# Optimization experiments

Hardware: AMD Instinct MI355X
Metric: run time of the kernel (lower is better)

The kernel has to match this reference:

```python
import jax, jax.numpy as jnp
import numpy as np
import math

B, S, D, H, DQ, DV, P = 8, 1024, 512, 8, 64, 64, 32


def _layer_norm(x, g, b, eps=1e-5):
    mu = jnp.mean(x, axis=-1, keepdims=True)
    var = jnp.mean((x - mu) ** 2, axis=-1, keepdims=True)
    return (x - mu) * jax.lax.rsqrt(var + eps) * g + b


def setup_inputs() -> dict:
    key = jax.random.key(0)
    ks = jax.random.split(key, 12)
    s = 0.02
    x = jax.random.normal(ks[0], (B, S, D), dtype=jnp.float32)
    lengths = jax.random.randint(ks[1], (B,), S // 2, S + 1)  # avoid fully-masked rows
    return {
        "x": x,
        "ln_g": jnp.ones((D,), jnp.float32),
        "ln_b": jnp.zeros((D,), jnp.float32),
        "Wk": jax.random.normal(ks[2], (D, H * DQ), jnp.float32) * s,
        "bk": jnp.zeros((H * DQ,), jnp.float32),
        "Wv": jax.random.normal(ks[3], (D, H * DV), jnp.float32) * s,
        "bv": jnp.zeros((H * DV,), jnp.float32),
        "pos": jax.random.normal(ks[4], (1, S, S, P), jnp.float32) * s,  # learned pos table
        "wp": jax.random.normal(ks[5], (P,), jnp.float32) * s,  # map_pos Linear(P,1) weight
        "bp": jnp.zeros((), jnp.float32),  # map_pos bias
        "Wo": jax.random.normal(ks[6], (H * DV, D), jnp.float32) * s,
        "bo": jnp.zeros((D,), jnp.float32),
        "key_value_sequence_lengths": lengths,
    }


def reference(x, ln_g, ln_b, Wk, bk, Wv, bv, pos, wp, bp, Wo, bo, key_value_sequence_lengths):
    # self-attention, encoder (no causal mask), 'kv+pos' branch, eval mode (dropout off)
    xn = _layer_norm(x, ln_g, ln_b)
    k = (xn @ Wk + bk).reshape(B, S, H, DQ).transpose(0, 2, 1, 3)  # [B,H,S,DQ]
    v = (xn @ Wv + bv).reshape(B, S, H, DV).transpose(0, 2, 1, 3)  # [B,H,S,DV]

    # kv+pos: scores use keys twice (tmp = keys since N == M)
    scores = jnp.einsum("bhnd,bhmd->bhnm", k, k) / math.sqrt(H)
    # map_pos(scores[...,None] + pos) == scores * sum(wp) + pos@wp + bp (linear, fused)
    bias = jnp.einsum("qkp,p->qk", pos[0], wp) + bp  # [S,S]
    attn = scores * jnp.sum(wp) + bias[None, None]
    attn = attn / math.sqrt(DQ)

    key_ok = jnp.arange(S)[None, None, None, :] < key_value_sequence_lengths[:, None, None, None]
    attn = jnp.where(key_ok, attn, -jnp.inf)
    probs = jax.nn.softmax(attn, axis=-1)  # [B,H,S,S]

    out = jnp.einsum("bhnm,bhmd->bhnd", probs, v)
    out = out.transpose(0, 2, 1, 3).reshape(B, S, H * DV)
    seq = out @ Wo + bo + x
    return seq, probs
```

## Files before the change

kernel.cpp:

```cpp
#include <hip/hip_runtime.h>
#include <hip/hip_bf16.h>


typedef __attribute__((ext_vector_type(8))) short short8;
typedef __attribute__((ext_vector_type(4))) short short4v;
typedef __attribute__((ext_vector_type(4))) float float4v;

#define MFMA16(a, b, c) __builtin_amdgcn_mfma_f32_16x16x32_bf16((a), (b), (c), 0, 0, 0)

__device__ inline unsigned short f2bf(float f) {
    unsigned u = __builtin_bit_cast(unsigned, f);
    unsigned r = (u + 0x7FFFu + ((u >> 16) & 1u)) >> 16;
    return (unsigned short)r;
}
__device__ inline float bf2f(unsigned short h) {
    unsigned u = ((unsigned)h) << 16;
    return __builtin_bit_cast(float, u);
}

__device__ __forceinline__ void async16(const void* g, void* l) {
    __builtin_amdgcn_global_load_lds(
        (const __attribute__((address_space(1))) unsigned int*)(unsigned long long)g,
        (__attribute__((address_space(3))) unsigned int*)(unsigned)(unsigned long long)l,
        16, 0, 0);
}

__device__ __forceinline__ void barrier_lds() {
    asm volatile("s_waitcnt lgkmcnt(0)" ::: "memory");
    __builtin_amdgcn_sched_barrier(0);
    __builtin_amdgcn_s_barrier();
    __builtin_amdgcn_sched_barrier(0);
}

__global__ __launch_bounds__(256) void ln_kernel(const float* __restrict__ x,
                                                 const float* __restrict__ g,
                                                 const float* __restrict__ b,
                                                 unsigned short* __restrict__ xn) {
    int wave = threadIdx.x >> 6;
    int lane = threadIdx.x & 63;
    size_t row = (size_t)blockIdx.x * 4 + wave;
    const float4* x4 = (const float4*)(x + row * 512);
    float4 v0 = x4[lane];
    float4 v1 = x4[lane + 64];
    float s = v0.x + v0.y + v0.z + v0.w + v1.x + v1.y + v1.z + v1.w;
    for (int o = 32; o; o >>= 1) s += __shfl_xor(s, o);
    float mu = s * (1.0f / 512.0f);
    float d0x = v0.x - mu, d0y = v0.y - mu, d0z = v0.z - mu, d0w = v0.w - mu;
    float d1x = v1.x - mu, d1y = v1.y - mu, d1z = v1.z - mu, d1w = v1.w - mu;
    float q = d0x * d0x + d0y * d0y + d0z * d0z + d0w * d0w +
              d1x * d1x + d1y * d1y + d1z * d1z + d1w * d1w;
    for (int o = 32; o; o >>= 1) q += __shfl_xor(q, o);
    float rs = rsqrtf(q * (1.0f / 512.0f) + 1e-5f);
    const float4* g4 = (const float4*)g;
    const float4* b4 = (const float4*)b;
    float4 g0 = g4[lane], g1 = g4[lane + 64];
    float4 b0 = b4[lane], b1 = b4[lane + 64];
    short4v o0, o1;
    o0[0] = (short)f2bf(d0x * rs * g0.x + b0.x);
    o0[1] = (short)f2bf(d0y * rs * g0.y + b0.y);
    o0[2] = (short)f2bf(d0z * rs * g0.z + b0.z);
    o0[3] = (short)f2bf(d0w * rs * g0.w + b0.w);
    o1[0] = (short)f2bf(d1x * rs * g1.x + b1.x);
    o1[1] = (short)f2bf(d1y * rs * g1.y + b1.y);
    o1[2] = (short)f2bf(d1z * rs * g1.z + b1.z);
    o1[3] = (short)f2bf(d1w * rs * g1.w + b1.w);
    *(short4v*)(xn + row * 512 + lane * 4) = o0;
    *(short4v*)(xn + row * 512 + 256 + lane * 4) = o1;
}

__global__ __launch_bounds__(256) void wconv_kernel(const float* __restrict__ Wk,
                                                    const float* __restrict__ Wv,
                                                    const float* __restrict__ Wo,
                                                    unsigned short* __restrict__ WkT,
                                                    unsigned short* __restrict__ WvT,
                                                    unsigned short* __restrict__ WoT) {
    int i = blockIdx.x * 256 + threadIdx.x;
    const float* src = (blockIdx.y == 0) ? Wk : (blockIdx.y == 1) ? Wv : Wo;
    unsigned short* dst = (blockIdx.y == 0) ? WkT : (blockIdx.y == 1) ? WvT : WoT;
    int k = i >> 9, n = i & 511;
    dst[n * 512 + k] = f2bf(src[i]);
}

__global__ __launch_bounds__(256) void bias_kernel(const float* __restrict__ pos,
                                                   const float* __restrict__ wp,
                                                   const float* __restrict__ bp,
                                                   unsigned short* __restrict__ biasT) {
    int lane = threadIdx.x & 63;
    int w = threadIdx.x >> 6;
    size_t wbase = ((size_t)blockIdx.x * 4 + w) * 64;
    float4 wv = ((const float4*)wp)[lane & 7];
    float bias0 = bp[0];
#pragma unroll
    for (int t = 0; t < 8; t++) {
        size_t p0 = wbase + (size_t)t * 8;
        const float4* src = (const float4*)(pos + p0 * 32);
        float4 d = src[lane];
        float s = d.x * wv.x + d.y * wv.y + d.z * wv.z + d.w * wv.w;
        s += __shfl_xor(s, 1);
        s += __shfl_xor(s, 2);
        s += __shfl_xor(s, 4);
        if ((lane & 7) == 0) {
            size_t p = p0 + (lane >> 3);
            int q = (int)(p >> 10), k = (int)(p & 1023);
            biasT[(size_t)k * 1024 + q] = f2bf((s + bias0) * 0.125f);
        }
    }
}

__global__ __launch_bounds__(256) void proj_kernel(const unsigned short* __restrict__ xn,
                                                   const unsigned short* __restrict__ WkT,
                                                   const unsigned short* __restrict__ WvT,
                                                   const float* __restrict__ bk,
                                                   const float* __restrict__ bv,
                                                   unsigned short* __restrict__ K,
                                                   unsigned short* __restrict__ Vt) {
    __shared__ unsigned short sa[128 * 32];
    __shared__ unsigned short sb[128 * 32];
    int z = blockIdx.z;
    const unsigned short* Bm = z ? WvT : WkT;
    const float* bias = z ? bv : bk;
    int m0 = blockIdx.y * 128, n0 = blockIdx.x * 128;
    int lane = threadIdx.x & 63, w = threadIdx.x >> 6;
    int l15 = lane & 15, quad = lane >> 4, q8 = quad * 8;
    int wm = w >> 1, wn = w & 1;
    int srow = w * 16 + (lane >> 2);
    int scol = (lane & 3) * 8;
    float4v acc[4][4] = {};
    for (int k0 = 0; k0 < 512; k0 += 32) {
        __syncthreads();
        async16(xn + (size_t)(m0 + srow) * 512 + k0 + scol, &sa[w * 512]);
        async16(xn + (size_t)(m0 + 64 + srow) * 512 + k0 + scol, &sa[2048 + w * 512]);
        async16(Bm + (size_t)(n0 + srow) * 512 + k0 + scol, &sb[w * 512]);
        async16(Bm + (size_t)(n0 + 64 + srow) * 512 + k0 + scol, &sb[2048 + w * 512]);
        __syncthreads();
        short8 af[4], bf[4];
#pragma unroll
        for (int t = 0; t < 4; t++)
            af[t] = *(const short8*)&sa[(wm * 64 + t * 16 + l15) * 32 + q8];
#pragma unroll
        for (int t = 0; t < 4; t++)
            bf[t] = *(const short8*)&sb[(wn * 64 + t * 16 + l15) * 32 + q8];
#pragma unroll
        for (int mt = 0; mt < 4; mt++)
#pragma unroll
            for (int nt = 0; nt < 4; nt++)
                acc[mt][nt] = MFMA16(af[mt], bf[nt], acc[mt][nt]);
    }
#pragma unroll
    for (int mt = 0; mt < 4; mt++)
#pragma unroll
        for (int nt = 0; nt < 4; nt++)
#pragma unroll
            for (int r = 0; r < 4; r++) {
                int m = m0 + wm * 64 + mt * 16 + quad * 4 + r;
                int n = n0 + wn * 64 + nt * 16 + l15;
                float v = acc[mt][nt][r] + bias[n];
                int b = m >> 10, s = m & 1023;
                int h = n >> 6, d = n & 63;
                if (z == 0)
                    K[(((size_t)b * 8 + h) * 1024 + s) * 64 + d] = f2bf(v);
                else
                    Vt[(((size_t)b * 8 + h) * 64 + d) * 1024 + s] = f2bf(v);
            }
}

__global__ __launch_bounds__(256) void attn_kernel(const unsigned short* __restrict__ K,
                                                   const unsigned short* __restrict__ Vt,
                                                   const unsigned short* __restrict__ biasT,
                                                   const float* __restrict__ wp,
                                                   const int* __restrict__ lens,
                                                   float* __restrict__ probs,
                                                   unsigned short* __restrict__ outb) {
    __shared__ unsigned short sc[16 * 1032];
    int bid = blockIdx.x;
    int sup = bid >> 6, wi = bid & 63;
    int bh = (sup & ~7) | (wi >> 3);
    int qt = ((sup & 7) << 3) | (wi & 7);
    int b = bh >> 3, h = bh & 7;
    int q0 = qt * 16;
    int lane = threadIdx.x & 63;
    int w = threadIdx.x >> 6;
    int l15 = lane & 15, quad = lane >> 4;
    int q8 = quad * 8;
    int len = lens[b];

    float swp = 0.f;
#pragma unroll
    for (int j = 0; j < 32; j++) swp += wp[j];
    float c1 = swp * 0.04419417382415922f;

    const unsigned short* Kbh = K + (size_t)bh * 1024 * 64;
    short8 a00 = *(const short8*)(Kbh + (size_t)(q0 + l15) * 64 + q8);
    short8 a01 = *(const short8*)(Kbh + (size_t)(q0 + l15) * 64 + q8 + 32);

#pragma unroll 2
    for (int i = 0; i < 16; i++) {
        int n0 = (i * 4 + w) * 16;
        short8 b0 = *(const short8*)(Kbh + (size_t)(n0 + l15) * 64 + q8);
        short8 b1 = *(const short8*)(Kbh + (size_t)(n0 + l15) * 64 + q8 + 32);
        float4v acc0 = {};
        acc0 = MFMA16(a00, b0, acc0);
        acc0 = MFMA16(a01, b1, acc0);
        int key = n0 + l15;
        bool ok = key < len;
        short4v bb4 = *(const short4v*)(biasT + (size_t)key * 1024 + q0 + quad * 4);
#pragma unroll
        for (int r = 0; r < 4; r++) {
            int row0 = quad * 4 + r;
            float lg0 = ok ? acc0[r] * c1 + bf2f((unsigned short)bb4[r]) : -1e30f;
            sc[row0 * 1032 + key] = f2bf(lg0);
        }
    }
    barrier_lds();

    for (int rr = 0; rr < 4; rr++) {
        int row = w * 4 + rr;
        float v[16];
        float mx = -1e30f;
#pragma unroll
        for (int j = 0; j < 16; j++) {
            v[j] = bf2f(sc[row * 1032 + lane + j * 64]);
            mx = fmaxf(mx, v[j]);
        }
        for (int o = 32; o; o >>= 1) mx = fmaxf(mx, __shfl_xor(mx, o));
        float s = 0.f;
#pragma unroll
        for (int j = 0; j < 16; j++) {
            v[j] = __expf(v[j] - mx);
            s += v[j];
        }
        for (int o = 32; o; o >>= 1) s += __shfl_xor(s, o);
        float inv = 1.0f / s;
        float* prow = probs + ((size_t)bh * 1024 + q0 + row) * 1024;
#pragma unroll
        for (int j = 0; j < 16; j++) {
            float p = v[j] * inv;
            sc[row * 1032 + lane + j * 64] = f2bf(p);
            __builtin_nontemporal_store(p, prow + lane + j * 64);
        }
    }
    barrier_lds();

    int nv = w * 16;
    const unsigned short* Vbh = Vt + (size_t)bh * 64 * 1024;
    float4v o0a = {}, o0b = {};
    for (int ks = 0; ks < 32; ks += 2) {
        int k0 = ks * 32;
        short8 bb0 = *(const short8*)(Vbh + (size_t)(nv + l15) * 1024 + k0 + q8);
        short8 p0 = *(const short8*)&sc[l15 * 1032 + k0 + q8];
        short8 bb1 = *(const short8*)(Vbh + (size_t)(nv + l15) * 1024 + k0 + 32 + q8);
        short8 p1 = *(const short8*)&sc[l15 * 1032 + k0 + 32 + q8];
        o0a = MFMA16(p0, bb0, o0a);
        o0b = MFMA16(p1, bb1, o0b);
    }
    float4v o0 = o0a + o0b;
#pragma unroll
    for (int r = 0; r < 4; r++) {
        int row = quad * 4 + r;
        int qa = q0 + row;
        outb[((size_t)b * 1024 + qa) * 512 + h * 64 + nv + l15] = f2bf(o0[r]);
    }
}

__global__ __launch_bounds__(256) void oproj_kernel(const unsigned short* __restrict__ outb,
                                                    const unsigned short* __restrict__ WoT,
                                                    const float* __restrict__ bo,
                                                    const float* __restrict__ x,
                                                    float* __restrict__ seq) {
    __shared__ unsigned short sa[128 * 32];
    __shared__ unsigned short sb[128 * 32];
    int m0 = blockIdx.y * 128, n0 = blockIdx.x * 128;
    int lane = threadIdx.x & 63, w = threadIdx.x >> 6;
    int l15 = lane & 15, quad = lane >> 4, q8 = quad * 8;
    int wm = w >> 1, wn = w & 1;
    int srow = w * 16 + (lane >> 2);
    int scol = (lane & 3) * 8;
    float4v acc[4][4] = {};
    for (int k0 = 0; k0 < 512; k0 += 32) {
        __syncthreads();
        async16(outb + (size_t)(m0 + srow) * 512 + k0 + scol, &sa[w * 512]);
        async16(outb + (size_t)(m0 + 64 + srow) * 512 + k0 + scol, &sa[2048 + w * 512]);
        async16(WoT + (size_t)(n0 + srow) * 512 + k0 + scol, &sb[w * 512]);
        async16(WoT + (size_t)(n0 + 64 + srow) * 512 + k0 + scol, &sb[2048 + w * 512]);
        __syncthreads();
        short8 af[4], bf[4];
#pragma unroll
        for (int t = 0; t < 4; t++)
            af[t] = *(const short8*)&sa[(wm * 64 + t * 16 + l15) * 32 + q8];
#pragma unroll
        for (int t = 0; t < 4; t++)
            bf[t] = *(const short8*)&sb[(wn * 64 + t * 16 + l15) * 32 + q8];
#pragma unroll
        for (int mt = 0; mt < 4; mt++)
#pragma unroll
            for (int nt = 0; nt < 4; nt++)
                acc[mt][nt] = MFMA16(af[mt], bf[nt], acc[mt][nt]);
    }
#pragma unroll
    for (int mt = 0; mt < 4; mt++)
#pragma unroll
        for (int nt = 0; nt < 4; nt++)
#pragma unroll
            for (int r = 0; r < 4; r++) {
                int m = m0 + wm * 64 + mt * 16 + quad * 4 + r;
                int n = n0 + wn * 64 + nt * 16 + l15;
                seq[(size_t)m * 512 + n] = acc[mt][nt][r] + bo[n] + x[(size_t)m * 512 + n];
            }
}

extern "C" void kernel_launch(void* const* d_in, const int* in_sizes, int n_in,
                              void* d_out, int out_size, void* d_ws, size_t ws_size,
                              hipStream_t stream) {
    const float* x    = (const float*)d_in[0];
    const float* ln_g = (const float*)d_in[1];
    const float* ln_b = (const float*)d_in[2];
    const float* Wk   = (const float*)d_in[3];
    const float* bk   = (const float*)d_in[4];
    const float* Wv   = (const float*)d_in[5];
    const float* bv   = (const float*)d_in[6];
    const float* pos  = (const float*)d_in[7];
    const float* wp   = (const float*)d_in[8];
    const float* bp   = (const float*)d_in[9];
    const float* Wo   = (const float*)d_in[10];
    const float* bo   = (const float*)d_in[11];
    const int* lens   = (const int*)d_in[12];

    unsigned short* WkT  = (unsigned short*)d_ws;
    unsigned short* WvT  = WkT + 512 * 512;
    unsigned short* WoT  = WvT + 512 * 512;
    unsigned short* xn   = WoT + 512 * 512;
    unsigned short* Kb   = xn + (size_t)8192 * 512;
    unsigned short* Vt   = Kb + (size_t)64 * 1024 * 64;
    unsigned short* outb = Vt + (size_t)64 * 64 * 1024;
    unsigned short* biasT = outb + (size_t)8192 * 512;

    float* seq = (float*)d_out;
    float* probs = seq + (size_t)8192 * 512;

    hipLaunchKernelGGL(wconv_kernel, dim3(1024, 3), dim3(256), 0, stream,
                       Wk, Wv, Wo, WkT, WvT, WoT);
    hipLaunchKernelGGL(ln_kernel, dim3(2048), dim3(256), 0, stream, x, ln_g, ln_b, xn);
    hipLaunchKernelGGL(bias_kernel, dim3(4096), dim3(256), 0, stream, pos, wp, bp, biasT);
    hipLaunchKernelGGL(proj_kernel, dim3(4, 64, 2), dim3(256), 0, stream,
                       xn, WkT, WvT, bk, bv, Kb, Vt);
    hipLaunchKernelGGL(attn_kernel, dim3(4096), dim3(256), 0, stream,
                       Kb, Vt, biasT, wp, lens, probs, outb);
    hipLaunchKernelGGL(oproj_kernel, dim3(4, 64), dim3(256), 0, stream,
                       outb, WoT, bo, x, seq);
}
```

Before: 563.9 us.

## Keep attention logits in registers and transpose weights through LDS tiles

```diff
diff --git a/kernel.cpp b/kernel.cpp
--- a/kernel.cpp
+++ b/kernel.cpp
@@ -74,11 +74,24 @@
                                                     unsigned short* __restrict__ WkT,
                                                     unsigned short* __restrict__ WvT,
                                                     unsigned short* __restrict__ WoT) {
-    int i = blockIdx.x * 256 + threadIdx.x;
-    const float* src = (blockIdx.y == 0) ? Wk : (blockIdx.y == 1) ? Wv : Wo;
-    unsigned short* dst = (blockIdx.y == 0) ? WkT : (blockIdx.y == 1) ? WvT : WoT;
-    int k = i >> 9, n = i & 511;
-    dst[n * 512 + k] = f2bf(src[i]);
+    __shared__ unsigned short t[64 * 66];
+    int z = blockIdx.z;
+    const float* src = (z == 0) ? Wk : (z == 1) ? Wv : Wo;
+    unsigned short* dst = (z == 0) ? WkT : (z == 1) ? WvT : WoT;
+    int k0 = blockIdx.x * 64, n0 = blockIdx.y * 64;
+    int tx = threadIdx.x & 63, ty = threadIdx.x >> 6;
+#pragma unroll
+    for (int rr = 0; rr < 16; rr++) {
+        int k = ty * 16 + rr;
+        float v = src[(size_t)(k0 + k) * 512 + n0 + tx];
+        t[tx * 66 + k] = f2bf(v);
+    }
+    __syncthreads();
+#pragma unroll
+    for (int rr = 0; rr < 16; rr++) {
+        int n = ty * 16 + rr;
+        dst[(size_t)(n0 + n) * 512 + k0 + tx] = t[n * 66 + tx];
+    }
 }
 
 __global__ __launch_bounds__(256) void bias_kernel(const float* __restrict__ pos,
@@ -164,18 +177,17 @@
             }
 }
 
-__global__ __launch_bounds__(256) void attn_kernel(const unsigned short* __restrict__ K,
-                                                   const unsigned short* __restrict__ Vt,
-                                                   const unsigned short* __restrict__ biasT,
-                                                   const float* __restrict__ wp,
-                                                   const int* __restrict__ lens,
-                                                   float* __restrict__ probs,
-                                                   unsigned short* __restrict__ outb) {
+__global__ __launch_bounds__(256, 4) void attn_kernel(const unsigned short* __restrict__ K,
+                                                      const unsigned short* __restrict__ Vt,
+                                                      const unsigned short* __restrict__ biasT,
+                                                      const float* __restrict__ wp,
+                                                      const int* __restrict__ lens,
+                                                      float* __restrict__ probs,
+                                                      unsigned short* __restrict__ outb) {
     __shared__ unsigned short sc[16 * 1032];
+    __shared__ float red[2][4][16];
     int bid = blockIdx.x;
-    int sup = bid >> 6, wi = bid & 63;
-    int bh = (sup & ~7) | (wi >> 3);
-    int qt = ((sup & 7) << 3) | (wi & 7);
+    int bh = bid >> 6, qt = bid & 63;
     int b = bh >> 3, h = bh & 7;
     int q0 = qt * 16;
     int lane = threadIdx.x & 63;
@@ -193,50 +205,84 @@
     short8 a00 = *(const short8*)(Kbh + (size_t)(q0 + l15) * 64 + q8);
     short8 a01 = *(const short8*)(Kbh + (size_t)(q0 + l15) * 64 + q8 + 32);
 
-#pragma unroll 2
+    float4v lg[16];
+#pragma unroll
     for (int i = 0; i < 16; i++) {
         int n0 = (i * 4 + w) * 16;
-        short8 b0 = *(const short8*)(Kbh + (size_t)(n0 + l15) * 64 + q8);
-        short8 b1 = *(const short8*)(Kbh + (size_t)(n0 + l15) * 64 + q8 + 32);
-        float4v acc0 = {};
-        acc0 = MFMA16(a00, b0, acc0);
-        acc0 = MFMA16(a01, b1, acc0);
         int key = n0 + l15;
+        short8 b0 = *(const short8*)(Kbh + (size_t)key * 64 + q8);
+        short8 b1 = *(const short8*)(Kbh + (size_t)key * 64 + q8 + 32);
+        float4v acc = {};
+        acc = MFMA16(a00, b0, acc);
+        acc = MFMA16(a01, b1, acc);
+        short4v bb4 = *(const short4v*)(biasT + (size_t)key * 1024 + q0 + quad * 4);
         bool ok = key < len;
-        short4v bb4 = *(const short4v*)(biasT + (size_t)key * 1024 + q0 + quad * 4);
+#pragma unroll
+        for (int r = 0; r < 4; r++)
+            lg[i][r] = ok ? acc[r] * c1 + bf2f((unsigned short)bb4[r]) : -1e30f;
+    }
+
+    float mx[4];
+#pragma unroll
+    for (int r = 0; r < 4; r++) {
+        float m = lg[0][r];
+#pragma unroll
+        for (int i = 1; i < 16; i++) m = fmaxf(m, lg[i][r]);
+        m = fmaxf(m, __shfl_xor(m, 1));
+        m = fmaxf(m, __shfl_xor(m, 2));
+        m = fmaxf(m, __shfl_xor(m, 4));
+        m = fmaxf(m, __shfl_xor(m, 8));
+        mx[r] = m;
+    }
+    if (l15 < 4) {
+        float v = (l15 == 0) ? mx[0] : (l15 == 1) ? mx[1] : (l15 == 2) ? mx[2] : mx[3];
+        red[0][w][quad * 4 + l15] = v;
+    }
+    barrier_lds();
+#pragma unroll
+    for (int r = 0; r < 4; r++) {
+        int row = quad * 4 + r;
+        mx[r] = fmaxf(fmaxf(red[0][0][row], red[0][1][row]),
+                      fmaxf(red[0][2][row], red[0][3][row]));
+    }
+
+    float sm[4];
+#pragma unroll
+    for (int r = 0; r < 4; r++) {
+        float s = 0.f;
+#pragma unroll
+        for (int i = 0; i < 16; i++) {
+            float e = __expf(lg[i][r] - mx[r]);
+            lg[i][r] = e;
+            s += e;
+        }
+        s += __shfl_xor(s, 1);
+        s += __shfl_xor(s, 2);
+        s += __shfl_xor(s, 4);
+        s += __shfl_xor(s, 8);
+        sm[r] = s;
+    }
+    if (l15 < 4) {
+        float v = (l15 == 0) ? sm[0] : (l15 == 1) ? sm[1] : (l15 == 2) ? sm[2] : sm[3];
+        red[1][w][quad * 4 + l15] = v;
+    }
+    barrier_lds();
+    float inv[4];
+#pragma unroll
+    for (int r = 0; r < 4; r++) {
+        int row = quad * 4 + r;
+        inv[r] = 1.0f / (red[1][0][row] + red[1][1][row] + red[1][2][row] + red[1][3][row]);
+    }
+
+#pragma unroll
+    for (int i = 0; i < 16; i++) {
+        int key = (i * 4 + w) * 16 + l15;
 #pragma unroll
         for (int r = 0; r < 4; r++) {
-            int row0 = quad * 4 + r;
-            float lg0 = ok ? acc0[r] * c1 + bf2f((unsigned short)bb4[r]) : -1e30f;
-            sc[row0 * 1032 + key] = f2bf(lg0);
-        }
-    }
-    barrier_lds();
-
-    for (int rr = 0; rr < 4; rr++) {
-        int row = w * 4 + rr;
-        float v[16];
-        float mx = -1e30f;
-#pragma unroll
-        for (int j = 0; j < 16; j++) {
-            v[j] = bf2f(sc[row * 1032 + lane + j * 64]);
-            mx = fmaxf(mx, v[j]);
-        }
-        for (int o = 32; o; o >>= 1) mx = fmaxf(mx, __shfl_xor(mx, o));
-        float s = 0.f;
-#pragma unroll
-        for (int j = 0; j < 16; j++) {
-            v[j] = __expf(v[j] - mx);
-            s += v[j];
-        }
-        for (int o = 32; o; o >>= 1) s += __shfl_xor(s, o);
-        float inv = 1.0f / s;
-        float* prow = probs + ((size_t)bh * 1024 + q0 + row) * 1024;
-#pragma unroll
-        for (int j = 0; j < 16; j++) {
-            float p = v[j] * inv;
-            sc[row * 1032 + lane + j * 64] = f2bf(p);
-            __builtin_nontemporal_store(p, prow + lane + j * 64);
+            int row = quad * 4 + r;
+            float p = lg[i][r] * inv[r];
+            sc[row * 1032 + key] = f2bf(p);
+            __builtin_nontemporal_store(p, probs + ((size_t)bh * 1024 + q0 + row) * 1024 + key);
         }
     }
     barrier_lds();
@@ -249,7 +295,7 @@
         short8 bb0 = *(const short8*)(Vbh + (size_t)(nv + l15) * 1024 + k0 + q8);
         short8 p0 = *(const short8*)&sc[l15 * 1032 + k0 + q8];
         short8 bb1 = *(const short8*)(Vbh + (size_t)(nv + l15) * 1024 + k0 + 32 + q8);
-        short8 p1 = *(const short8*)&sc[l15 * 1032 + k0 + 32 + q8];
+        short8 p1 = *(const short8*)&sc[(l15)*1032 + k0 + 32 + q8];
         o0a = MFMA16(p0, bb0, o0a);
         o0b = MFMA16(p1, bb1, o0b);
     }
@@ -337,7 +383,7 @@
     float* seq = (float*)d_out;
     float* probs = seq + (size_t)8192 * 512;
 
-    hipLaunchKernelGGL(wconv_kernel, dim3(1024, 3), dim3(256), 0, stream,
+    hipLaunchKernelGGL(wconv_kernel, dim3(8, 8, 3), dim3(256), 0, stream,
                        Wk, Wv, Wo, WkT, WvT, WoT);
     hipLaunchKernelGGL(ln_kernel, dim3(2048), dim3(256), 0, stream, x, ln_g, ln_b, xn);
     hipLaunchKernelGGL(bias_kernel, dim3(4096), dim3(256), 0, stream, pos, wp, bp, biasT);
```

Result: no change. 561.8 us (-0.4%).
